# Kernel tuning notes

Hardware: AMD Instinct MI355X
Metric: run time of the kernel (lower is better)

## Reference

```python
import jax, jax.numpy as jnp
import numpy as np


def _conv2d(x, w, b, pad, rhs_dilation=(1, 1)):
    out = jax.lax.conv_general_dilated(
        x, w, window_strides=(1, 1),
        padding=((pad, pad), (pad, pad)),
        rhs_dilation=rhs_dilation,
        dimension_numbers=('NCHW', 'OIHW', 'NCHW'))
    return out + b[None, :, None, None]


def _bilinear(img, gx, gy):
    # img [C,H,W]; gx,gy [9,h,w] in [-1,1]; grid_sample bilinear, align_corners=True.
    # Coords are pre-clamped to [-1,1] so all samples are in-bounds; clamped
    # neighbor indices get zero bilinear weight at the boundary, matching torch.
    C, H, W = img.shape
    ix = (gx + 1.0) * 0.5 * (W - 1)
    iy = (gy + 1.0) * 0.5 * (H - 1)
    x0 = jnp.floor(ix)
    y0 = jnp.floor(iy)
    wx = ix - x0
    wy = iy - y0
    x0i = jnp.clip(x0.astype(jnp.int32), 0, W - 1)
    x1i = jnp.clip(x0i + 1, 0, W - 1)
    y0i = jnp.clip(y0.astype(jnp.int32), 0, H - 1)
    y1i = jnp.clip(y0i + 1, 0, H - 1)
    v00 = img[:, y0i, x0i]
    v01 = img[:, y0i, x1i]
    v10 = img[:, y1i, x0i]
    v11 = img[:, y1i, x1i]
    return (v00 * (1 - wx) * (1 - wy) + v01 * wx * (1 - wy)
            + v10 * (1 - wx) * wy + v11 * wx * wy)  # [C,9,h,w]


def _forward(x, conv_w, conv_b, offset_w, offset_b, mod_w, mod_b):
    b, c, h, w = x.shape
    offset = _conv2d(x, offset_w, offset_b, pad=1)          # [b,18,h,w]
    gx = jnp.clip(offset[:, :9] + jnp.linspace(-1.0, 1.0, w)[None, None, None, :], -1.0, 1.0)
    gy = jnp.clip(offset[:, 9:] + jnp.linspace(-1.0, 1.0, h)[None, None, :, None], -1.0, 1.0)
    sampled = jax.vmap(_bilinear)(x, gx, gy)                # [b,c,9,h,w]
    mod = _conv2d(x, mod_w, mod_b, pad=1)                   # [b,9,h,w]
    interp = sampled * mod[:, None]                         # [b,c,9,h,w]
    # tile the 9 samples into a 3h x 3w spatial grid: sample k = i + j*3 goes to block (j, i)
    tiled = interp.reshape(b, c, 3, 3, h, w).transpose(0, 1, 2, 4, 3, 5).reshape(b, c, 3 * h, 3 * w)
    # dilated 3x3 conv with dilation (h+1, w+1), stride 1, padding 1 -> [b,oc,h,w]
    return _conv2d(tiled, conv_w, conv_b, pad=1, rhs_dilation=(h + 1, w + 1))


def setup_inputs() -> dict:
    key = jax.random.key(0)
    ks = jax.random.split(key, 7)
    B, C, OC, H, W = 8, 256, 256, 64, 64
    return {
        'x': jax.random.normal(ks[0], (B, C, H, W), jnp.float32),
        'conv_w': jax.random.normal(ks[1], (OC, C, 3, 3), jnp.float32) * 0.02,
        'conv_b': jax.random.normal(ks[2], (OC,), jnp.float32) * 0.02,
        'offset_w': jax.random.normal(ks[3], (18, C, 3, 3), jnp.float32) * 0.01,
        'offset_b': jax.random.normal(ks[4], (18,), jnp.float32) * 0.01,
        'mod_w': jax.random.normal(ks[5], (9, C, 3, 3), jnp.float32) * 0.02,
        'mod_b': jax.random.normal(ks[6], (9,), jnp.float32) * 0.02,
    }


def reference(x, conv_w, conv_b, offset_w, offset_b, mod_w, mod_b):
    return _forward(x, conv_w, conv_b, offset_w, offset_b, mod_w, mod_b)
```

## Files before the change

### kernel.cpp

```cpp
#include <hip/hip_runtime.h>

typedef __attribute__((ext_vector_type(8))) _Float16 f16x8;
typedef __attribute__((ext_vector_type(4))) float f32x4;

#define CB 8
#define CC 256
#define CHW 4096


__global__ __launch_bounds__(256) void pxk(const float* __restrict__ x,
                                           const float* __restrict__ convw,
                                           const float* __restrict__ offw,
                                           const float* __restrict__ modw,
                                           _Float16* __restrict__ wAf,
                                           _Float16* __restrict__ wAomF,
                                           _Float16* __restrict__ xt) {
    __shared__ ushort tile[64][136];
    int bid = blockIdx.x;
    int tid = threadIdx.x;

    if (bid < 288) {
        int i = bid * 256 + tid;
        {
            int lane = i & 63, tl = (i >> 6) & 15, cc = (i >> 10) & 7, t = i >> 13;
            int oc = tl * 16 + (lane & 15);
            int cb = cc * 32 + (lane >> 4) * 8;
            f16x8 v;
#pragma unroll
            for (int j = 0; j < 8; ++j)
                v[j] = (_Float16)convw[oc * 2304 + (cb + j) * 9 + t];
            *(f16x8*)(wAf + (size_t)i * 8) = v;
        }
        if (i < 9216) {
            int lane = i & 63, tl = (i >> 6) & 1, cc = (i >> 7) & 7, t = i >> 10;
            int mr = tl * 16 + (lane & 15);
            int cb = cc * 32 + (lane >> 4) * 8;
            f16x8 u;
#pragma unroll
            for (int j = 0; j < 8; ++j) {
                int c = cb + j;
                float vv = 0.f;
                if (mr < 18) vv = offw[(mr * 256 + c) * 9 + t];
                else if (mr < 27) vv = modw[((mr - 18) * 256 + c) * 9 + t];
                u[j] = (_Float16)vv;
            }
            *(f16x8*)(wAomF + (size_t)i * 8) = u;
        }
        return;
    }

    int nb = bid - 288;
    int b = nb & 7, g = nb >> 3;
    int pos0 = (g >> 1) << 6;
    int ch0 = (g & 1) << 7;
    int p = tid & 63;
    const float* xb = x + ((size_t)b << 20);
#pragma unroll 4
    for (int rep = 0; rep < 32; rep++) {
        int c = ch0 + rep * 4 + (tid >> 6);
        _Float16 h = (_Float16)xb[((size_t)c << 12) + pos0 + p];
        tile[p][c - ch0] = __builtin_bit_cast(ushort, h);
    }
    __syncthreads();
    _Float16* xtb = xt + ((size_t)b << 20);
#pragma unroll
    for (int rep = 0; rep < 4; rep++) {
        int item = rep * 256 + tid;
        int pp = item >> 4, c16 = item & 15;
        f16x8 v = *(const f16x8*)((const char*)&tile[0][0] + pp * 272 + c16 * 16);
        *(f16x8*)((char*)xtb + (((size_t)(pos0 + pp)) << 9) + (ch0 << 1) + (c16 << 4)) = v;
    }
}

__global__ __launch_bounds__(128) void k1(const _Float16* __restrict__ xt,
                                          const _Float16* __restrict__ wAomF,
                                          const float* __restrict__ offb,
                                          const float* __restrict__ modb,
                                          float4* __restrict__ descW,
                                          int4* __restrict__ descO) {
    __shared__ float sEp[32][36];

    int bid = blockIdx.x;
    int b = bid & 7, yx = bid >> 3;
    int y = yx >> 1, xh = yx & 1;
    int tid = threadIdx.x;
    int lane = tid & 63;
    int w = __builtin_amdgcn_readfirstlane(tid >> 6);
    int l15 = lane & 15, oct = lane >> 4;

    const _Float16* xtb = xt + ((size_t)b << 20);
    int kylo = (y == 0) ? 1 : 0;
    int kyhi = (y == 63) ? 1 : 2;

    f32x4 acc[2];
    acc[0] = (f32x4)0.f;
    acc[1] = (f32x4)0.f;
    f16x8 Z = {};

    int pxl = (w << 4) + l15;
    int px = (xh << 5) + pxl;

    for (int ty = kylo; ty <= kyhi; ++ty) {
        int yy = y + ty - 1;
#pragma unroll
        for (int tx = 0; tx < 3; ++tx) {
            int t = ty * 3 + tx;
            int xx = px + tx - 1;
            bool val = (xx >= 0 && xx < 64);
            int xxc = min(max(xx, 0), 63);
            const f16x8* bp = (const f16x8*)(xtb + (((yy << 6) + xxc) << 8) + oct * 8);
            const f16x8* wf = (const f16x8*)wAomF + (size_t)t * 16 * 64 + lane;
#pragma unroll
            for (int c0 = 0; c0 < 256; c0 += 32) {
                f16x8 bf = bp[c0 >> 3];
                if (!val) bf = Z;
                int cc = c0 >> 5;
#pragma unroll
                for (int m = 0; m < 2; m++) {
                    f16x8 af = wf[(cc * 2 + m) * 64];
                    acc[m] = __builtin_amdgcn_mfma_f32_16x16x32_f16(af, bf, acc[m], 0, 0, 0);
                }
            }
        }
    }

#pragma unroll
    for (int m = 0; m < 2; m++) {
#pragma unroll
        for (int r = 0; r < 4; r++) {
            int row = (m << 4) + (oct << 2) + r;
            if (row < 27) sEp[row][pxl] = acc[m][r];
        }
    }
    __syncthreads();

    int gq = tid >> 5;
    int xl = tid & 31;
    if (gq < 3) {
        int xx2 = (xh << 5) + xl;
        float lx = -1.0f + xx2 * (2.0f / 63.0f);
        float ly = -1.0f + y * (2.0f / 63.0f);
#pragma unroll
        for (int j = 0; j < 3; j++) {
            int k = gq * 3 + j;
            float gx = sEp[k][xl] + offb[k] + lx;
            gx = fminf(fmaxf(gx, -1.f), 1.f);
            float gy = sEp[9 + k][xl] + offb[9 + k] + ly;
            gy = fminf(fmaxf(gy, -1.f), 1.f);
            float m = sEp[18 + k][xl] + modb[k];
            float ix = (gx + 1.0f) * 0.5f * 63.0f;
            float iy = (gy + 1.0f) * 0.5f * 63.0f;
            float fx = floorf(ix), fy = floorf(iy);
            float wx = ix - fx, wy = iy - fy;
            int x0 = min(max((int)fx, 0), 63);
            int x1 = min(x0 + 1, 63);
            int y0 = min(max((int)fy, 0), 63);
            int y1 = min(y0 + 1, 63);
            float w00 = (1.f - wx) * (1.f - wy) * m;
            float w01 = wx * (1.f - wy) * m;
            float w10 = (1.f - wx) * wy * m;
            float w11 = wx * wy * m;
            int di = ((b * 9 + k) << 12) + (y << 6) + xx2;
            descW[di] = make_float4(w00, w01, w10, w11);
            descO[di] = make_int4(((y0 << 6) + x0) << 9, ((y0 << 6) + x1) << 9,
                                  ((y1 << 6) + x0) << 9, ((y1 << 6) + x1) << 9);
        }
    }
}

__global__ __launch_bounds__(512, 4) void k2(const _Float16* __restrict__ xt,
                                             const _Float16* __restrict__ wAf,
                                             const float4* __restrict__ descW,
                                             const int4* __restrict__ descO,
                                             const float* __restrict__ convb,
                                             float* __restrict__ out) {
    __shared__ char cmb[2][8192];
    __shared__ float4 sDW[2][64];
    __shared__ int sDO[2][256];

    int bid = blockIdx.x;
    int b = bid & 7, oy = bid >> 3;
    int tid = threadIdx.x;
    int l = tid & 63;
    int wid = __builtin_amdgcn_readfirstlane(tid >> 6);
    int oct = l >> 4, l15 = l & 15;

    const char* xtb = (const char*)(xt + ((size_t)b << 20));

    f32x4 acc[2][4];
#pragma unroll
    for (int mt = 0; mt < 2; mt++)
#pragma unroll
        for (int nt = 0; nt < 4; nt++) acc[mt][nt] = (f32x4)0.f;

    int p_ox = (tid >> 3) & 63;
    int p_cs = tid & 7;
    int csl = (p_ox << 7) + ((p_cs ^ (p_ox & 7)) << 4);

    auto stage_desc = [&](int t) {
        int slot = t & 1;
        int xx = tid;
        int ky = t / 3, kx = t % 3;
        int yy = oy + ky - 1;
        int xp = xx + kx - 1;
        float4 w4s = make_float4(0.f, 0.f, 0.f, 0.f);
        int4 o4 = make_int4(0, 0, 0, 0);
        if (yy >= 0 && yy < 64 && xp >= 0 && xp < 64) {
            int di = ((b * 9 + t) << 12) + (yy << 6) + xp;
            w4s = descW[di];
            o4 = descO[di];
        }
        sDW[slot][xx] = w4s;
        sDO[slot][xx * 4 + 0] = o4.x;
        sDO[slot][xx * 4 + 1] = o4.y;
        sDO[slot][xx * 4 + 2] = o4.z;
        sDO[slot][xx * 4 + 3] = o4.w;
    };

    f16x8 cr[4];
    float4 w4;

    auto load_corners = [&](int t, int q) {
        int slot = t & 1;
        const int* dof = &sDO[slot][p_ox * 4];
        w4 = sDW[slot][p_ox];
#pragma unroll
        for (int c = 0; c < 4; ++c)
            cr[c] = *(const f16x8*)(xtb + dof[c] + q * 128 + p_cs * 16);
    };

    auto write_cmb = [&](int nb) {
        _Float16 h0 = (_Float16)w4.x, h1 = (_Float16)w4.y;
        _Float16 h2 = (_Float16)w4.z, h3 = (_Float16)w4.w;
        f16x8 W0 = {h0, h0, h0, h0, h0, h0, h0, h0};
        f16x8 W1 = {h1, h1, h1, h1, h1, h1, h1, h1};
        f16x8 W2 = {h2, h2, h2, h2, h2, h2, h2, h2};
        f16x8 W3 = {h3, h3, h3, h3, h3, h3, h3, h3};
        f16x8 r = cr[0] * W0 + cr[1] * W1 + cr[2] * W2 + cr[3] * W3;
        *(f16x8*)(cmb[nb] + csl) = r;
    };

    if (tid < 64) stage_desc(0);
    __syncthreads();
    load_corners(0, 0);
    write_cmb(0);
    __syncthreads();

    for (int p = 0; p < 36; ++p) {
        int t = p >> 2, q = p & 3, pb = p & 1;
        bool hasNext = (p + 1 < 36);

        f16x8 afr[2][2];
        {
            const f16x8* wf = (const f16x8*)wAf +
                              ((size_t)((t * 8 + q * 2) * 16) + wid * 2) * 64 + l;
            afr[0][0] = wf[0];
            afr[0][1] = wf[64];
            afr[1][0] = wf[16 * 64];
            afr[1][1] = wf[17 * 64];
        }

        if (hasNext) load_corners((p + 1) >> 2, (p + 1) & 3);
        if (q == 0 && t + 1 < 9 && tid < 64) stage_desc(t + 1);

        const char* src = cmb[pb];
        __builtin_amdgcn_s_setprio(1);
#pragma unroll
        for (int ks2 = 0; ks2 < 2; ++ks2) {
            f16x8 bfr[4];
            int cs = (ks2 << 2) + oct;
#pragma unroll
            for (int nt = 0; nt < 4; ++nt) {
                int ox = (nt << 4) + l15;
                bfr[nt] = *(const f16x8*)(src + (ox << 7) + ((cs ^ (ox & 7)) << 4));
            }
#pragma unroll
            for (int mt = 0; mt < 2; ++mt)
#pragma unroll
                for (int nt = 0; nt < 4; ++nt)
                    acc[mt][nt] = __builtin_amdgcn_mfma_f32_16x16x32_f16(
                        afr[ks2][mt], bfr[nt], acc[mt][nt], 0, 0, 0);
        }
        __builtin_amdgcn_s_setprio(0);

        if (hasNext) write_cmb(pb ^ 1);
        __syncthreads();
    }

    size_t outb = ((size_t)b << 20);
#pragma unroll
    for (int mt = 0; mt < 2; ++mt) {
#pragma unroll
        for (int nt = 0; nt < 4; ++nt) {
            int ox = (nt << 4) + l15;
#pragma unroll
            for (int r = 0; r < 4; ++r) {
                int oc = (wid << 5) + (mt << 4) + (oct << 2) + r;
                out[outb + (size_t)oc * 4096 + (oy << 6) + ox] = acc[mt][nt][r] + convb[oc];
            }
        }
    }
}

extern "C" void kernel_launch(void* const* d_in, const int* in_sizes, int n_in,
                              void* d_out, int out_size, void* d_ws, size_t ws_size,
                              hipStream_t stream) {
    const float* x     = (const float*)d_in[0];
    const float* convw = (const float*)d_in[1];
    const float* convb = (const float*)d_in[2];
    const float* offw  = (const float*)d_in[3];
    const float* offb  = (const float*)d_in[4];
    const float* modw  = (const float*)d_in[5];
    const float* modb  = (const float*)d_in[6];
    float* out = (float*)d_out;

    char* ws = (char*)d_ws;
    _Float16* wAf   = (_Float16*)(ws);
    _Float16* wAomF = (_Float16*)(ws + 1179648);
    float4*   descW = (float4*)(ws + 1327104);
    int4*     descO = (int4*)(ws + 6045696);
    _Float16* xt    = (_Float16*)(ws + 10764288);

    hipLaunchKernelGGL(pxk, dim3(1312), dim3(256), 0, stream, x, convw, offw, modw, wAf, wAomF, xt);
    hipLaunchKernelGGL(k1, dim3(1024), dim3(128), 0, stream, xt, wAomF, offb, modb, descW, descO);
    hipLaunchKernelGGL(k2, dim3(512), dim3(512), 0, stream, xt, wAf, descW, descO, convb, out);
}
```

Baseline: 98.88 us.

## Deepen corner-gather prefetch to two steps with double register buffers

Restructures the main loop of k2 so the bilinear corner gathers for step P+2 are issued while step P runs its MFMAs. Two register buffer sets alternate, and the loop is unrolled by two. Descriptors are now stored as int4 in shared memory and read once per tap into registers, and the B-fragment LDS offsets are precomputed. The s_setprio hints are dropped. The aim is to hide global gather latency behind compute, at the cost of more VGPRs, which may lower occupancy.

```diff
diff --git a/kernel.cpp b/kernel.cpp
--- a/kernel.cpp
+++ b/kernel.cpp
@@ -176,7 +176,7 @@
                                              float* __restrict__ out) {
     __shared__ char cmb[2][8192];
     __shared__ float4 sDW[2][64];
-    __shared__ int sDO[2][256];
+    __shared__ int4 sDO[2][64];
 
     int bid = blockIdx.x;
     int b = bid & 7, oy = bid >> 3;
@@ -196,13 +196,16 @@
     int p_ox = (tid >> 3) & 63;
     int p_cs = tid & 7;
     int csl = (p_ox << 7) + ((p_cs ^ (p_ox & 7)) << 4);
+    const char* xtb_cs = xtb + p_cs * 16;
+
+    int bofs0 = (l15 << 7) + ((oct ^ (l15 & 7)) << 4);
+    int bofs1 = (l15 << 7) + (((oct + 4) ^ (l15 & 7)) << 4);
 
     auto stage_desc = [&](int t) {
         int slot = t & 1;
-        int xx = tid;
         int ky = t / 3, kx = t % 3;
         int yy = oy + ky - 1;
-        int xp = xx + kx - 1;
+        int xp = tid + kx - 1;
         float4 w4s = make_float4(0.f, 0.f, 0.f, 0.f);
         int4 o4 = make_int4(0, 0, 0, 0);
         if (yy >= 0 && yy < 64 && xp >= 0 && xp < 64) {
@@ -210,81 +213,99 @@
             w4s = descW[di];
             o4 = descO[di];
         }
-        sDW[slot][xx] = w4s;
-        sDO[slot][xx * 4 + 0] = o4.x;
-        sDO[slot][xx * 4 + 1] = o4.y;
-        sDO[slot][xx * 4 + 2] = o4.z;
-        sDO[slot][xx * 4 + 3] = o4.w;
-    };
-
-    f16x8 cr[4];
-    float4 w4;
-
-    auto load_corners = [&](int t, int q) {
+        sDW[slot][tid] = w4s;
+        sDO[slot][tid] = o4;
+    };
+
+    int rdo0, rdo1, rdo2, rdo3;
+    _Float16 rh0, rh1, rh2, rh3;
+    auto refresh_desc = [&](int t) {
         int slot = t & 1;
-        const int* dof = &sDO[slot][p_ox * 4];
-        w4 = sDW[slot][p_ox];
-#pragma unroll
-        for (int c = 0; c < 4; ++c)
-            cr[c] = *(const f16x8*)(xtb + dof[c] + q * 128 + p_cs * 16);
-    };
-
-    auto write_cmb = [&](int nb) {
-        _Float16 h0 = (_Float16)w4.x, h1 = (_Float16)w4.y;
-        _Float16 h2 = (_Float16)w4.z, h3 = (_Float16)w4.w;
-        f16x8 W0 = {h0, h0, h0, h0, h0, h0, h0, h0};
-        f16x8 W1 = {h1, h1, h1, h1, h1, h1, h1, h1};
-        f16x8 W2 = {h2, h2, h2, h2, h2, h2, h2, h2};
-        f16x8 W3 = {h3, h3, h3, h3, h3, h3, h3, h3};
+        int4 o4 = sDO[slot][p_ox];
+        rdo0 = o4.x; rdo1 = o4.y; rdo2 = o4.z; rdo3 = o4.w;
+        float4 w4 = sDW[slot][p_ox];
+        rh0 = (_Float16)w4.x; rh1 = (_Float16)w4.y;
+        rh2 = (_Float16)w4.z; rh3 = (_Float16)w4.w;
+    };
+
+    f16x8 crA[4], crB[4];
+    _Float16 rcA[4], rcB[4];
+
+    auto issue_G = [&](f16x8* cr, _Float16* rc, int q) {
+        const char* base = xtb_cs + (q << 7);
+        cr[0] = *(const f16x8*)(base + rdo0);
+        cr[1] = *(const f16x8*)(base + rdo1);
+        cr[2] = *(const f16x8*)(base + rdo2);
+        cr[3] = *(const f16x8*)(base + rdo3);
+        rc[0] = rh0; rc[1] = rh1; rc[2] = rh2; rc[3] = rh3;
+    };
+
+    auto combine = [&](const f16x8* cr, const _Float16* rc, char* dst) {
+        f16x8 W0 = {rc[0], rc[0], rc[0], rc[0], rc[0], rc[0], rc[0], rc[0]};
+        f16x8 W1 = {rc[1], rc[1], rc[1], rc[1], rc[1], rc[1], rc[1], rc[1]};
+        f16x8 W2 = {rc[2], rc[2], rc[2], rc[2], rc[2], rc[2], rc[2], rc[2]};
+        f16x8 W3 = {rc[3], rc[3], rc[3], rc[3], rc[3], rc[3], rc[3], rc[3]};
         f16x8 r = cr[0] * W0 + cr[1] * W1 + cr[2] * W2 + cr[3] * W3;
-        *(f16x8*)(cmb[nb] + csl) = r;
+        *(f16x8*)(dst + csl) = r;
+    };
+
+    auto load_afr = [&](f16x8* afr, int p) {
+        int t = p >> 2, q = p & 3;
+        const f16x8* wf = (const f16x8*)wAf +
+                          ((size_t)((t * 8 + q * 2) * 16) + wid * 2) * 64 + l;
+        afr[0] = wf[0];
+        afr[1] = wf[64];
+        afr[2] = wf[16 * 64];
+        afr[3] = wf[17 * 64];
+    };
+
+    auto do_mfma = [&](const char* src, const f16x8* afr) {
+#pragma unroll
+        for (int ks2 = 0; ks2 < 2; ++ks2) {
+            f16x8 bfr[4];
+            int bofs = ks2 ? bofs1 : bofs0;
+#pragma unroll
+            for (int nt = 0; nt < 4; ++nt)
+                bfr[nt] = *(const f16x8*)(src + bofs + (nt << 11));
+#pragma unroll
+            for (int mt = 0; mt < 2; ++mt)
+#pragma unroll
+                for (int nt = 0; nt < 4; ++nt)
+                    acc[mt][nt] = __builtin_amdgcn_mfma_f32_16x16x32_f16(
+                        afr[ks2 * 2 + mt], bfr[nt], acc[mt][nt], 0, 0, 0);
+        }
     };
 
     if (tid < 64) stage_desc(0);
     __syncthreads();
-    load_corners(0, 0);
-    write_cmb(0);
+    refresh_desc(0);
+    issue_G(crA, rcA, 0);
+    combine(crA, rcA, cmb[0]);
+    issue_G(crA, rcA, 1);
     __syncthreads();
 
-    for (int p = 0; p < 36; ++p) {
-        int t = p >> 2, q = p & 3, pb = p & 1;
-        bool hasNext = (p + 1 < 36);
-
-        f16x8 afr[2][2];
+    f16x8 afr[4];
+#pragma unroll 1
+    for (int PP = 0; PP < 18; ++PP) {
         {
-            const f16x8* wf = (const f16x8*)wAf +
-                              ((size_t)((t * 8 + q * 2) * 16) + wid * 2) * 64 + l;
-            afr[0][0] = wf[0];
-            afr[0][1] = wf[64];
-            afr[1][0] = wf[16 * 64];
-            afr[1][1] = wf[17 * 64];
-        }
-
-        if (hasNext) load_corners((p + 1) >> 2, (p + 1) & 3);
-        if (q == 0 && t + 1 < 9 && tid < 64) stage_desc(t + 1);
-
-        const char* src = cmb[pb];
-        __builtin_amdgcn_s_setprio(1);
-#pragma unroll
-        for (int ks2 = 0; ks2 < 2; ++ks2) {
-            f16x8 bfr[4];
-            int cs = (ks2 << 2) + oct;
-#pragma unroll
-            for (int nt = 0; nt < 4; ++nt) {
-                int ox = (nt << 4) + l15;
-                bfr[nt] = *(const f16x8*)(src + (ox << 7) + ((cs ^ (ox & 7)) << 4));
-            }
-#pragma unroll
-            for (int mt = 0; mt < 2; ++mt)
-#pragma unroll
-                for (int nt = 0; nt < 4; ++nt)
-                    acc[mt][nt] = __builtin_amdgcn_mfma_f32_16x16x32_f16(
-                        afr[ks2][mt], bfr[nt], acc[mt][nt], 0, 0, 0);
-        }
-        __builtin_amdgcn_s_setprio(0);
-
-        if (hasNext) write_cmb(pb ^ 1);
-        __syncthreads();
+            int P = 2 * PP;
+            if (((P + 2) & 3) == 0 && P + 2 < 36) refresh_desc((P + 2) >> 2);
+            if (P + 2 < 36) issue_G(crB, rcB, (P + 2) & 3);
+            load_afr(afr, P);
+            if ((P & 3) == 0 && (P >> 2) + 1 < 9 && tid < 64) stage_desc((P >> 2) + 1);
+            do_mfma(cmb[P & 1], afr);
+            if (P + 1 < 36) combine(crA, rcA, cmb[(P + 1) & 1]);
+            __syncthreads();
+        }
+        {
+            int P = 2 * PP + 1;
+            if (((P + 2) & 3) == 0 && P + 2 < 36) refresh_desc((P + 2) >> 2);
+            if (P + 2 < 36) issue_G(crA, rcA, (P + 2) & 3);
+            load_afr(afr, P);
+            do_mfma(cmb[P & 1], afr);
+            if (P + 1 < 36) combine(crB, rcB, cmb[(P + 1) & 1]);
+            __syncthreads();
+        }
     }
 
     size_t outb = ((size_t)b << 20);
```

Result: slower. 128.0 us (+29.5%).
